# Optimization experiments

Measured on AMD Instinct MI355X. Metric: run time of the kernel, lower is better.

The kernel has to match this reference:

```python
import jax, jax.numpy as jnp
import numpy as np


def _split_box(v):
    # BoxTensor.from_vector: split last dim into (min z, max Z)
    D = v.shape[-1] // 2
    return v[..., :D], v[..., D:]


def setup_inputs() -> dict:
    key = jax.random.key(0)
    k1, k2 = jax.random.split(key)
    men_embeds = jax.random.normal(k1, (256, 128), dtype=jnp.float32)
    all_en_embeds = jax.random.normal(k2, (20000, 128), dtype=jnp.float32)
    return {"men_embeds": men_embeds, "all_en_embeds": all_en_embeds}


def reference(men_embeds, all_en_embeds):
    # men boxes: [M, D] min/max ; entity boxes: [N, D] min/max
    zm, Zm = _split_box(men_embeds)
    ze, Ze = _split_box(all_en_embeds)
    # intersection box per (mention, candidate): [M, N, D]
    lo = jnp.maximum(zm[:, None, :], ze[None, :, :])
    hi = jnp.minimum(Zm[:, None, :], Ze[None, :, :])
    # soft volume: prod_d softplus(side) -> log-volume = sum log softplus
    log_int_vol = jnp.sum(jnp.log(jax.nn.softplus(hi - lo)), axis=-1)   # [M, N]
    log_men_vol = jnp.sum(jnp.log(jax.nn.softplus(Zm - zm)), axis=-1)   # [M]
    # containment log prob = log vol(men ∩ en) - log vol(men); logits = exp(.)
    return jnp.exp(log_int_vol - log_men_vol[:, None])
```

## Files before the change

### kernel.cpp

```cpp
#include <hip/hip_runtime.h>


#define BM 32
#define BN 64
#define DD 64
#define MST 34
#define NST 68
#define CLEN 8
#define NCHUNK 8

__global__ __launch_bounds__(256, 3)
void ivr_kernel(const float* __restrict__ men, const float* __restrict__ en,
                float* __restrict__ out, int M, int N) {
    __shared__ __align__(16) float sEm[DD][MST];
    __shared__ __align__(16) float sIm[DD][MST];
    __shared__ __align__(16) float sEe[DD][NST];
    __shared__ __align__(16) float sIe[DD][NST];
    __shared__ float sRc[NCHUNK][MST];

    const int tx = threadIdx.x;
    const int m0 = blockIdx.y * BM;
    const int n0 = blockIdx.x * BN;

    {
        const int m = tx >> 3;
        const int c = tx & 7;
        int mm = m0 + m; if (mm >= M) mm = M - 1;
        const float* row = men + (size_t)mm * 128;
        float prod = 1.0f;
        #pragma unroll
        for (int k = 0; k < CLEN; ++k) {
            const int d = c * CLEN + k;
            const float Em = __expf(row[DD + d]);
            const float Im = __expf(-row[d]);
            sEm[d][m] = Em;
            sIm[d][m] = Im;
            prod *= __log2f(1.0f + Em * Im);
        }
        sRc[c][m] = 1.0f / prod;
    }
    for (int i = tx; i < BN * DD; i += 256) {
        const int d = i & (DD - 1);
        const int n = i >> 6;
        int nn = n0 + n; if (nn >= N) nn = N - 1;
        sEe[d][n] = __expf(en[(size_t)nn * 128 + DD + d]);
        sIe[d][n] = __expf(-en[(size_t)nn * 128 + d]);
    }
    __syncthreads();

    const int ni = (tx & 15) * 4;
    const int mi = (tx >> 4) * 2;

    float p[2][4];
    #pragma unroll
    for (int i = 0; i < 2; ++i)
        #pragma unroll
        for (int j = 0; j < 4; ++j) p[i][j] = 1.0f;

    #pragma unroll 1
    for (int c = 0; c < NCHUNK; ++c) {
        #pragma unroll
        for (int k = 0; k < CLEN; ++k) {
            const int d = c * CLEN + k;
            const float2 Em2 = *reinterpret_cast<const float2*>(&sEm[d][mi]);
            const float2 Im2 = *reinterpret_cast<const float2*>(&sIm[d][mi]);
            const float4 Ee4 = *reinterpret_cast<const float4*>(&sEe[d][ni]);
            const float4 Ie4 = *reinterpret_cast<const float4*>(&sIe[d][ni]);
            const float EmA[2] = {Em2.x, Em2.y};
            const float ImA[2] = {Im2.x, Im2.y};
            const float EeA[4] = {Ee4.x, Ee4.y, Ee4.z, Ee4.w};
            const float IeA[4] = {Ie4.x, Ie4.y, Ie4.z, Ie4.w};
            #pragma unroll
            for (int i = 0; i < 2; ++i) {
                #pragma unroll
                for (int j = 0; j < 4; ++j) {
                    const float u = fminf(EmA[i], EeA[j]) * fminf(ImA[i], IeA[j]);
                    p[i][j] *= __log2f(1.0f + u);
                }
            }
        }
        const float rc0 = sRc[c][mi];
        const float rc1 = sRc[c][mi + 1];
        #pragma unroll
        for (int j = 0; j < 4; ++j) { p[0][j] *= rc0; p[1][j] *= rc1; }
    }

    #pragma unroll
    for (int i = 0; i < 2; ++i) {
        const int m = m0 + mi + i;
        if (m >= M) continue;
        const int n = n0 + ni;
        if (n + 4 <= N) {
            *reinterpret_cast<float4*>(&out[(size_t)m * N + n]) =
                make_float4(p[i][0], p[i][1], p[i][2], p[i][3]);
        } else {
            #pragma unroll
            for (int j = 0; j < 4; ++j)
                if (n + j < N) out[(size_t)m * N + n + j] = p[i][j];
        }
    }
}

extern "C" void kernel_launch(void* const* d_in, const int* in_sizes, int n_in,
                              void* d_out, int out_size, void* d_ws, size_t ws_size,
                              hipStream_t stream) {
    const float* men = (const float*)d_in[0];
    const float* en  = (const float*)d_in[1];
    float* out = (float*)d_out;
    const int M = in_sizes[0] / 128;
    const int N = in_sizes[1] / 128;
    dim3 grid((N + BN - 1) / BN, (M + BM - 1) / BM);
    ivr_kernel<<<grid, dim3(256), 0, stream>>>(men, en, out, M, N);
}
```

Baseline: 143.3 us.

## Split depth into halves, shrink shared memory, process two N tiles per block

Staging now covers the feature dimension in two halves of 32, which roughly halves shared memory per block, and the launch bounds are raised from 3 to 5 blocks per CU. Each block now loops over two N tiles with a stride, so the grid is about half as wide. Global loads become float4, and log2(1+u) is computed with fmaf. The intent is more occupancy and fewer blocks to launch. The cost is an extra sync pair per half, mention boxes recomputed for every half and tile, and possible register pressure under the tighter bound.

```diff
diff --git a/kernel.cpp b/kernel.cpp
--- a/kernel.cpp
+++ b/kernel.cpp
@@ -3,100 +3,129 @@
 
 #define BM 32
 #define BN 64
-#define DD 64
+#define DH 32
 #define MST 34
-#define NST 68
-#define CLEN 8
-#define NCHUNK 8
+#define NST 66
 
-__global__ __launch_bounds__(256, 3)
+__global__ __launch_bounds__(256, 5)
 void ivr_kernel(const float* __restrict__ men, const float* __restrict__ en,
-                float* __restrict__ out, int M, int N) {
-    __shared__ __align__(16) float sEm[DD][MST];
-    __shared__ __align__(16) float sIm[DD][MST];
-    __shared__ __align__(16) float sEe[DD][NST];
-    __shared__ __align__(16) float sIe[DD][NST];
-    __shared__ float sRc[NCHUNK][MST];
+                float* __restrict__ out, int M, int N, int ntl, int jst) {
+    __shared__ float sEm[DH][MST];
+    __shared__ float sIm[DH][MST];
+    __shared__ float sEe[DH][NST];
+    __shared__ float sIe[DH][NST];
+    __shared__ float sRc[4][MST];
 
     const int tx = threadIdx.x;
     const int m0 = blockIdx.y * BM;
-    const int n0 = blockIdx.x * BN;
-
-    {
-        const int m = tx >> 3;
-        const int c = tx & 7;
-        int mm = m0 + m; if (mm >= M) mm = M - 1;
-        const float* row = men + (size_t)mm * 128;
-        float prod = 1.0f;
-        #pragma unroll
-        for (int k = 0; k < CLEN; ++k) {
-            const int d = c * CLEN + k;
-            const float Em = __expf(row[DD + d]);
-            const float Im = __expf(-row[d]);
-            sEm[d][m] = Em;
-            sIm[d][m] = Im;
-            prod *= __log2f(1.0f + Em * Im);
-        }
-        sRc[c][m] = 1.0f / prod;
-    }
-    for (int i = tx; i < BN * DD; i += 256) {
-        const int d = i & (DD - 1);
-        const int n = i >> 6;
-        int nn = n0 + n; if (nn >= N) nn = N - 1;
-        sEe[d][n] = __expf(en[(size_t)nn * 128 + DD + d]);
-        sIe[d][n] = __expf(-en[(size_t)nn * 128 + d]);
-    }
-    __syncthreads();
+    const int j  = blockIdx.x;
 
     const int ni = (tx & 15) * 4;
     const int mi = (tx >> 4) * 2;
 
-    float p[2][4];
-    #pragma unroll
-    for (int i = 0; i < 2; ++i)
+    const int ntiles = (j + jst < ntl) ? 2 : 1;
+
+    for (int t = 0; t < ntiles; ++t) {
+        const int n0 = (j + t * jst) * BN;
+
+        float p[2][4];
         #pragma unroll
-        for (int j = 0; j < 4; ++j) p[i][j] = 1.0f;
+        for (int i = 0; i < 2; ++i)
+            #pragma unroll
+            for (int jj = 0; jj < 4; ++jj) p[i][jj] = 1.0f;
 
-    #pragma unroll 1
-    for (int c = 0; c < NCHUNK; ++c) {
         #pragma unroll
-        for (int k = 0; k < CLEN; ++k) {
-            const int d = c * CLEN + k;
-            const float2 Em2 = *reinterpret_cast<const float2*>(&sEm[d][mi]);
-            const float2 Im2 = *reinterpret_cast<const float2*>(&sIm[d][mi]);
-            const float4 Ee4 = *reinterpret_cast<const float4*>(&sEe[d][ni]);
-            const float4 Ie4 = *reinterpret_cast<const float4*>(&sIe[d][ni]);
-            const float EmA[2] = {Em2.x, Em2.y};
-            const float ImA[2] = {Im2.x, Im2.y};
-            const float EeA[4] = {Ee4.x, Ee4.y, Ee4.z, Ee4.w};
-            const float IeA[4] = {Ie4.x, Ie4.y, Ie4.z, Ie4.w};
+        for (int h = 0; h < 2; ++h) {
+            const int dofs = h * DH;
+
+            if (tx < 128) {
+                const int m = tx & 31;
+                const int c = tx >> 5;
+                int mm = m0 + m; if (mm >= M) mm = M - 1;
+                const float* row = men + (size_t)mm * 128 + dofs + c * 8;
+                const float4 za = *reinterpret_cast<const float4*>(row);
+                const float4 zb = *reinterpret_cast<const float4*>(row + 4);
+                const float4 Za = *reinterpret_cast<const float4*>(row + 64);
+                const float4 Zb = *reinterpret_cast<const float4*>(row + 68);
+                const float zA[8] = {za.x, za.y, za.z, za.w, zb.x, zb.y, zb.z, zb.w};
+                const float ZA[8] = {Za.x, Za.y, Za.z, Za.w, Zb.x, Zb.y, Zb.z, Zb.w};
+                float prod = 1.0f;
+                #pragma unroll
+                for (int k = 0; k < 8; ++k) {
+                    const int dl = c * 8 + k;
+                    const float Em = __expf(ZA[k]);
+                    const float Im = __expf(-zA[k]);
+                    sEm[dl][m] = Em;
+                    sIm[dl][m] = Im;
+                    prod *= __log2f(fmaf(Em, Im, 1.0f));
+                }
+                sRc[c][m] = 1.0f / prod;
+            }
             #pragma unroll
-            for (int i = 0; i < 2; ++i) {
+            for (int it = 0; it < 2; ++it) {
+                const int q   = tx + it * 256;
+                const int dl4 = (q & 7) * 4;
+                const int n   = q >> 3;
+                int nn = n0 + n; if (nn >= N) nn = N - 1;
+                const float* erow = en + (size_t)nn * 128 + dofs + dl4;
+                const float4 z4 = *reinterpret_cast<const float4*>(erow);
+                const float4 Z4 = *reinterpret_cast<const float4*>(erow + 64);
+                sEe[dl4 + 0][n] = __expf(Z4.x);
+                sEe[dl4 + 1][n] = __expf(Z4.y);
+                sEe[dl4 + 2][n] = __expf(Z4.z);
+                sEe[dl4 + 3][n] = __expf(Z4.w);
+                sIe[dl4 + 0][n] = __expf(-z4.x);
+                sIe[dl4 + 1][n] = __expf(-z4.y);
+                sIe[dl4 + 2][n] = __expf(-z4.z);
+                sIe[dl4 + 3][n] = __expf(-z4.w);
+            }
+            __syncthreads();
+
+            #pragma unroll 1
+            for (int c = 0; c < 4; ++c) {
                 #pragma unroll
-                for (int j = 0; j < 4; ++j) {
-                    const float u = fminf(EmA[i], EeA[j]) * fminf(ImA[i], IeA[j]);
-                    p[i][j] *= __log2f(1.0f + u);
+                for (int k = 0; k < 8; ++k) {
+                    const int dl = c * 8 + k;
+                    const float2 Em2 = *reinterpret_cast<const float2*>(&sEm[dl][mi]);
+                    const float2 Im2 = *reinterpret_cast<const float2*>(&sIm[dl][mi]);
+                    const float2 Ee0 = *reinterpret_cast<const float2*>(&sEe[dl][ni]);
+                    const float2 Ee1 = *reinterpret_cast<const float2*>(&sEe[dl][ni + 2]);
+                    const float2 Ie0 = *reinterpret_cast<const float2*>(&sIe[dl][ni]);
+                    const float2 Ie1 = *reinterpret_cast<const float2*>(&sIe[dl][ni + 2]);
+                    const float EmA[2] = {Em2.x, Em2.y};
+                    const float ImA[2] = {Im2.x, Im2.y};
+                    const float EeA[4] = {Ee0.x, Ee0.y, Ee1.x, Ee1.y};
+                    const float IeA[4] = {Ie0.x, Ie0.y, Ie1.x, Ie1.y};
+                    #pragma unroll
+                    for (int i = 0; i < 2; ++i) {
+                        #pragma unroll
+                        for (int jj = 0; jj < 4; ++jj) {
+                            const float w = fmaf(fminf(EmA[i], EeA[jj]),
+                                                 fminf(ImA[i], IeA[jj]), 1.0f);
+                            p[i][jj] *= __log2f(w);
+                        }
+                    }
                 }
+                const float2 rc = *reinterpret_cast<const float2*>(&sRc[c][mi]);
+                #pragma unroll
+                for (int jj = 0; jj < 4; ++jj) { p[0][jj] *= rc.x; p[1][jj] *= rc.y; }
             }
+            __syncthreads();
         }
-        const float rc0 = sRc[c][mi];
-        const float rc1 = sRc[c][mi + 1];
+
         #pragma unroll
-        for (int j = 0; j < 4; ++j) { p[0][j] *= rc0; p[1][j] *= rc1; }
-    }
-
-    #pragma unroll
-    for (int i = 0; i < 2; ++i) {
-        const int m = m0 + mi + i;
-        if (m >= M) continue;
-        const int n = n0 + ni;
-        if (n + 4 <= N) {
-            *reinterpret_cast<float4*>(&out[(size_t)m * N + n]) =
-                make_float4(p[i][0], p[i][1], p[i][2], p[i][3]);
-        } else {
-            #pragma unroll
-            for (int j = 0; j < 4; ++j)
-                if (n + j < N) out[(size_t)m * N + n + j] = p[i][j];
+        for (int i = 0; i < 2; ++i) {
+            const int m = m0 + mi + i;
+            if (m >= M) continue;
+            const int n = n0 + ni;
+            if (n + 4 <= N) {
+                *reinterpret_cast<float4*>(&out[(size_t)m * N + n]) =
+                    make_float4(p[i][0], p[i][1], p[i][2], p[i][3]);
+            } else {
+                #pragma unroll
+                for (int jj = 0; jj < 4; ++jj)
+                    if (n + jj < N) out[(size_t)m * N + n + jj] = p[i][jj];
+            }
         }
     }
 }
@@ -109,6 +138,8 @@
     float* out = (float*)d_out;
     const int M = in_sizes[0] / 128;
     const int N = in_sizes[1] / 128;
-    dim3 grid((N + BN - 1) / BN, (M + BM - 1) / BM);
-    ivr_kernel<<<grid, dim3(256), 0, stream>>>(men, en, out, M, N);
+    const int ntl = (N + BN - 1) / BN;
+    const int jst = (ntl + 1) / 2;
+    dim3 grid(jst, (M + BM - 1) / BM);
+    ivr_kernel<<<grid, dim3(256), 0, stream>>>(men, en, out, M, N, ntl, jst);
 }
```

New measurement: 149.0 us. +4.0%, slower.

## Precompute exp-transformed boxes in workspace and stream tiles via LDS DMA

Applied to the files above, without the earlier changes.

Adds a pre-pass kernel that computes the exp-transformed entity and mention box bounds once, stored in tile-transposed layout in the workspace, along with the per-chunk reciprocal mention volumes. The main kernel then loads these tiles into shared memory with direct global-to-LDS loads, splits D into two halves to cut shared memory use and allow higher occupancy, and has each block handle two N tiles so mention data is reused. The goal is to stop recomputing exp for every (M-tile, N-tile) pair and to cut global-load latency. In exchange it adds a second launch and workspace traffic, and it falls back to the old kernel when the workspace is too small or M is not a multiple of 32.

```diff
diff --git a/kernel.cpp b/kernel.cpp
--- a/kernel.cpp
+++ b/kernel.cpp
@@ -1,27 +1,192 @@
 #include <hip/hip_runtime.h>
+#include <stdint.h>
 
 
 #define BM 32
 #define BN 64
-#define DD 64
-#define MST 34
-#define NST 68
-#define CLEN 8
-#define NCHUNK 8
+#define DH 32
+
+__device__ __forceinline__ void dma16(const float* g, float* l) {
+    __builtin_amdgcn_global_load_lds(
+        (const __attribute__((address_space(1))) void*)g,
+        (__attribute__((address_space(3))) void*)l, 16, 0, 0);
+}
+
+__global__ __launch_bounds__(256)
+void ivr_pre(const float* __restrict__ men, const float* __restrict__ en,
+             float* __restrict__ ws, int M, int N, int ntl) {
+    float* EeT = ws;
+    float* IeT = EeT + (size_t)ntl * 4096;
+    float* EmT = IeT + (size_t)ntl * 4096;
+    float* ImT = EmT + 16384;
+    float* RcG = ImT + 16384;
+    const int b = blockIdx.x, tx = threadIdx.x;
+    if (b < ntl) {
+        const int n0 = b * BN;
+        #pragma unroll
+        for (int i = 0; i < 8; ++i) {
+            const int q = i * 256 + tx;
+            const int n = q >> 5, c4 = q & 31;
+            int nn = n0 + n; if (nn >= N) nn = N - 1;
+            const float4 v = *reinterpret_cast<const float4*>(en + (size_t)nn * 128 + c4 * 4);
+            const float vv[4] = {v.x, v.y, v.z, v.w};
+            #pragma unroll
+            for (int e = 0; e < 4; ++e) {
+                const int d = c4 * 4 + e;
+                if (d < 64) {
+                    IeT[(size_t)b * 4096 + (d >> 5) * 2048 + (d & 31) * 64 + n] = __expf(-vv[e]);
+                } else {
+                    const int dd = d - 64;
+                    EeT[(size_t)b * 4096 + (dd >> 5) * 2048 + (dd & 31) * 64 + n] = __expf(vv[e]);
+                }
+            }
+        }
+    } else {
+        int m = tx; if (m >= M) m = M - 1;
+        const int mt = m >> 5, ml = m & 31;
+        const float* row = men + (size_t)m * 128;
+        float prod[8];
+        #pragma unroll
+        for (int c = 0; c < 8; ++c) prod[c] = 1.0f;
+        #pragma unroll
+        for (int c4 = 0; c4 < 16; ++c4) {
+            const float4 zv = *reinterpret_cast<const float4*>(row + c4 * 4);
+            const float4 Zv = *reinterpret_cast<const float4*>(row + 64 + c4 * 4);
+            const float zz[4] = {zv.x, zv.y, zv.z, zv.w};
+            const float ZZ[4] = {Zv.x, Zv.y, Zv.z, Zv.w};
+            #pragma unroll
+            for (int e = 0; e < 4; ++e) {
+                const int d = c4 * 4 + e;
+                const float Em = __expf(ZZ[e]);
+                const float Im = __expf(-zz[e]);
+                const int idx = (mt * 2 + (d >> 5)) * 1024 + (d & 31) * 32 + ml;
+                EmT[idx] = Em;
+                ImT[idx] = Im;
+                prod[d >> 3] *= __log2f(fmaf(Em, Im, 1.0f));
+            }
+        }
+        #pragma unroll
+        for (int c = 0; c < 8; ++c)
+            RcG[mt * 256 + c * 32 + ml] = 1.0f / prod[c];
+    }
+}
+
+__global__ __launch_bounds__(256, 6)
+void ivr_main(const float* __restrict__ ws, float* __restrict__ out,
+              int M, int N, int ntl, int jst) {
+    __shared__ __align__(16) float sEe[DH][BN];
+    __shared__ __align__(16) float sIe[DH][BN];
+    __shared__ __align__(16) float sEm[DH][BM];
+    __shared__ __align__(16) float sIm[DH][BM];
+    __shared__ __align__(16) float sRc[8][BM];
+
+    const float* EeT = ws;
+    const float* IeT = EeT + (size_t)ntl * 4096;
+    const float* EmT = IeT + (size_t)ntl * 4096;
+    const float* ImT = EmT + 16384;
+    const float* RcG = ImT + 16384;
+
+    const int tx = threadIdx.x;
+    const int w = tx >> 6, lane = tx & 63;
+    const int mt = blockIdx.y, j = blockIdx.x;
+    const int ntiles = (j + jst < ntl) ? 2 : 1;
+    const int ni = (tx & 15) * 4;
+    const int mi = (tx >> 4) * 2;
+
+    if (w == 0) dma16(RcG + mt * 256 + lane * 4, &sRc[0][0]);
+
+    float p[2][2][4];
+    #pragma unroll
+    for (int t = 0; t < 2; ++t)
+        #pragma unroll
+        for (int i = 0; i < 2; ++i)
+            #pragma unroll
+            for (int jj = 0; jj < 4; ++jj) p[t][i][jj] = 1.0f;
+
+    #pragma unroll 1
+    for (int h = 0; h < 2; ++h) {
+        {
+            const float* gEm = EmT + (mt * 2 + h) * 1024;
+            const float* gIm = ImT + (mt * 2 + h) * 1024;
+            dma16(gEm + w * 256 + lane * 4, &sEm[0][0] + w * 256);
+            dma16(gIm + w * 256 + lane * 4, &sIm[0][0] + w * 256);
+        }
+        for (int t = 0; t < ntiles; ++t) {
+            const int j2 = j + t * jst;
+            const float* gE = EeT + (size_t)j2 * 4096 + h * 2048;
+            const float* gI = IeT + (size_t)j2 * 4096 + h * 2048;
+            const int o = w * 512 + lane * 4;
+            dma16(gE + o,       &sEe[0][0] + w * 512);
+            dma16(gE + o + 256, &sEe[0][0] + w * 512 + 256);
+            dma16(gI + o,       &sIe[0][0] + w * 512);
+            dma16(gI + o + 256, &sIe[0][0] + w * 512 + 256);
+            __syncthreads();
+
+            #pragma unroll 1
+            for (int c = 0; c < 4; ++c) {
+                #pragma unroll
+                for (int k = 0; k < 8; ++k) {
+                    const int dl = c * 8 + k;
+                    const float2 Em2 = *reinterpret_cast<const float2*>(&sEm[dl][mi]);
+                    const float2 Im2 = *reinterpret_cast<const float2*>(&sIm[dl][mi]);
+                    const float4 Ee4 = *reinterpret_cast<const float4*>(&sEe[dl][ni]);
+                    const float4 Ie4 = *reinterpret_cast<const float4*>(&sIe[dl][ni]);
+                    const float EmA[2] = {Em2.x, Em2.y};
+                    const float ImA[2] = {Im2.x, Im2.y};
+                    const float EeA[4] = {Ee4.x, Ee4.y, Ee4.z, Ee4.w};
+                    const float IeA[4] = {Ie4.x, Ie4.y, Ie4.z, Ie4.w};
+                    #pragma unroll
+                    for (int i = 0; i < 2; ++i) {
+                        #pragma unroll
+                        for (int jj = 0; jj < 4; ++jj) {
+                            const float ww = fmaf(fminf(EmA[i], EeA[jj]),
+                                                  fminf(ImA[i], IeA[jj]), 1.0f);
+                            p[t][i][jj] *= __log2f(ww);
+                        }
+                    }
+                }
+                const float2 rc = *reinterpret_cast<const float2*>(&sRc[h * 4 + c][mi]);
+                #pragma unroll
+                for (int jj = 0; jj < 4; ++jj) { p[t][0][jj] *= rc.x; p[t][1][jj] *= rc.y; }
+            }
+            __syncthreads();
+        }
+    }
+
+    for (int t = 0; t < ntiles; ++t) {
+        const int n0 = (j + t * jst) * BN;
+        #pragma unroll
+        for (int i = 0; i < 2; ++i) {
+            const int m = mt * BM + mi + i;
+            if (m >= M) continue;
+            const int n = n0 + ni;
+            if (n + 4 <= N) {
+                *reinterpret_cast<float4*>(&out[(size_t)m * N + n]) =
+                    make_float4(p[t][i][0], p[t][i][1], p[t][i][2], p[t][i][3]);
+            } else {
+                #pragma unroll
+                for (int jj = 0; jj < 4; ++jj)
+                    if (n + jj < N) out[(size_t)m * N + n + jj] = p[t][i][jj];
+            }
+        }
+    }
+}
+
+#define FB_MST 34
+#define FB_NST 68
 
 __global__ __launch_bounds__(256, 3)
-void ivr_kernel(const float* __restrict__ men, const float* __restrict__ en,
-                float* __restrict__ out, int M, int N) {
-    __shared__ __align__(16) float sEm[DD][MST];
-    __shared__ __align__(16) float sIm[DD][MST];
-    __shared__ __align__(16) float sEe[DD][NST];
-    __shared__ __align__(16) float sIe[DD][NST];
-    __shared__ float sRc[NCHUNK][MST];
+void ivr_fb(const float* __restrict__ men, const float* __restrict__ en,
+            float* __restrict__ out, int M, int N) {
+    __shared__ __align__(16) float sEm[64][FB_MST];
+    __shared__ __align__(16) float sIm[64][FB_MST];
+    __shared__ __align__(16) float sEe[64][FB_NST];
+    __shared__ __align__(16) float sIe[64][FB_NST];
+    __shared__ float sRc[8][FB_MST];
 
     const int tx = threadIdx.x;
     const int m0 = blockIdx.y * BM;
     const int n0 = blockIdx.x * BN;
-
     {
         const int m = tx >> 3;
         const int c = tx & 7;
@@ -29,62 +194,61 @@
         const float* row = men + (size_t)mm * 128;
         float prod = 1.0f;
         #pragma unroll
-        for (int k = 0; k < CLEN; ++k) {
-            const int d = c * CLEN + k;
-            const float Em = __expf(row[DD + d]);
+        for (int k = 0; k < 8; ++k) {
+            const int d = c * 8 + k;
+            const float Em = __expf(row[64 + d]);
             const float Im = __expf(-row[d]);
             sEm[d][m] = Em;
             sIm[d][m] = Im;
-            prod *= __log2f(1.0f + Em * Im);
+            prod *= __log2f(fmaf(Em, Im, 1.0f));
         }
         sRc[c][m] = 1.0f / prod;
     }
-    for (int i = tx; i < BN * DD; i += 256) {
-        const int d = i & (DD - 1);
+    for (int i = tx; i < BN * 64; i += 256) {
+        const int d = i & 63;
         const int n = i >> 6;
         int nn = n0 + n; if (nn >= N) nn = N - 1;
-        sEe[d][n] = __expf(en[(size_t)nn * 128 + DD + d]);
+        sEe[d][n] = __expf(en[(size_t)nn * 128 + 64 + d]);
         sIe[d][n] = __expf(-en[(size_t)nn * 128 + d]);
     }
     __syncthreads();
 
     const int ni = (tx & 15) * 4;
     const int mi = (tx >> 4) * 2;
-
     float p[2][4];
     #pragma unroll
     for (int i = 0; i < 2; ++i)
         #pragma unroll
-        for (int j = 0; j < 4; ++j) p[i][j] = 1.0f;
+        for (int jj = 0; jj < 4; ++jj) p[i][jj] = 1.0f;
 
     #pragma unroll 1
-    for (int c = 0; c < NCHUNK; ++c) {
-        #pragma unroll
-        for (int k = 0; k < CLEN; ++k) {
-            const int d = c * CLEN + k;
+    for (int c = 0; c < 8; ++c) {
+        #pragma unroll
+        for (int k = 0; k < 8; ++k) {
+            const int d = c * 8 + k;
             const float2 Em2 = *reinterpret_cast<const float2*>(&sEm[d][mi]);
             const float2 Im2 = *reinterpret_cast<const float2*>(&sIm[d][mi]);
-            const float4 Ee4 = *reinterpret_cast<const float4*>(&sEe[d][ni]);
-            const float4 Ie4 = *reinterpret_cast<const float4*>(&sIe[d][ni]);
+            const float2 Ee0 = *reinterpret_cast<const float2*>(&sEe[d][ni]);
+            const float2 Ee1 = *reinterpret_cast<const float2*>(&sEe[d][ni + 2]);
+            const float2 Ie0 = *reinterpret_cast<const float2*>(&sIe[d][ni]);
+            const float2 Ie1 = *reinterpret_cast<const float2*>(&sIe[d][ni + 2]);
             const float EmA[2] = {Em2.x, Em2.y};
             const float ImA[2] = {Im2.x, Im2.y};
-            const float EeA[4] = {Ee4.x, Ee4.y, Ee4.z, Ee4.w};
-            const float IeA[4] = {Ie4.x, Ie4.y, Ie4.z, Ie4.w};
-            #pragma unroll
-            for (int i = 0; i < 2; ++i) {
-                #pragma unroll
-                for (int j = 0; j < 4; ++j) {
-                    const float u = fminf(EmA[i], EeA[j]) * fminf(ImA[i], IeA[j]);
-                    p[i][j] *= __log2f(1.0f + u);
+            const float EeA[4] = {Ee0.x, Ee0.y, Ee1.x, Ee1.y};
+            const float IeA[4] = {Ie0.x, Ie0.y, Ie1.x, Ie1.y};
+            #pragma unroll
+            for (int i = 0; i < 2; ++i)
+                #pragma unroll
+                for (int jj = 0; jj < 4; ++jj) {
+                    const float ww = fmaf(fminf(EmA[i], EeA[jj]),
+                                          fminf(ImA[i], IeA[jj]), 1.0f);
+                    p[i][jj] *= __log2f(ww);
                 }
-            }
-        }
-        const float rc0 = sRc[c][mi];
-        const float rc1 = sRc[c][mi + 1];
-        #pragma unroll
-        for (int j = 0; j < 4; ++j) { p[0][j] *= rc0; p[1][j] *= rc1; }
-    }
-
+        }
+        const float2 rc = *reinterpret_cast<const float2*>(&sRc[c][mi]);
+        #pragma unroll
+        for (int jj = 0; jj < 4; ++jj) { p[0][jj] *= rc.x; p[1][jj] *= rc.y; }
+    }
     #pragma unroll
     for (int i = 0; i < 2; ++i) {
         const int m = m0 + mi + i;
@@ -95,8 +259,8 @@
                 make_float4(p[i][0], p[i][1], p[i][2], p[i][3]);
         } else {
             #pragma unroll
-            for (int j = 0; j < 4; ++j)
-                if (n + j < N) out[(size_t)m * N + n + j] = p[i][j];
+            for (int jj = 0; jj < 4; ++jj)
+                if (n + jj < N) out[(size_t)m * N + n + jj] = p[i][jj];
         }
     }
 }
@@ -109,6 +273,13 @@
     float* out = (float*)d_out;
     const int M = in_sizes[0] / 128;
     const int N = in_sizes[1] / 128;
-    dim3 grid((N + BN - 1) / BN, (M + BM - 1) / BM);
-    ivr_kernel<<<grid, dim3(256), 0, stream>>>(men, en, out, M, N);
-}
+    const int ntl = (N + BN - 1) / BN;
+    const int jst = (ntl + 1) / 2;
+    const size_t need = ((size_t)2 * ntl * 4096 + 2 * 16384 + 2048) * sizeof(float);
+    if (ws_size >= need && (M & 31) == 0) {
+        ivr_pre<<<dim3(ntl + 1), dim3(256), 0, stream>>>(men, en, (float*)d_ws, M, N, ntl);
+        ivr_main<<<dim3(jst, M / BM), dim3(256), 0, stream>>>((const float*)d_ws, out, M, N, ntl, jst);
+    } else {
+        ivr_fb<<<dim3(ntl, (M + BM - 1) / BM), dim3(256), 0, stream>>>(men, en, out, M, N);
+    }
+}
```

Result: slower. 167.0 us (+16.5%).

## Bound intersections in fp16, zero negligible outputs, and compute only survivors exactly

Applied to the files above, without the earlier changes.

Replaces the single dense kernel with three passes. A stats pass computes per-mention reciprocal volumes and a cutoff. A cheap packed-fp16 bound pass sums the clipped side lengths per (mention, entity) pair and writes zeros. Pairs whose concavity-based upper bound exceeds the cutoff are appended to an atomic queue in workspace, and an exact pass recomputes only those pairs in fp32. This avoids the transcendental-heavy log/softplus work for the many pairs whose result is negligibly small. The cost is two extra launches, an atomic queue, and a silent cap on queue size. Outputs below roughly 2^-43.5 become exact zeros, and fp16 rounding could slightly loosen the bound.

```diff
diff --git a/kernel.cpp b/kernel.cpp
--- a/kernel.cpp
+++ b/kernel.cpp
@@ -1,103 +1,293 @@
 #include <hip/hip_runtime.h>
+#include <stdint.h>
 
 
 #define BM 32
 #define BN 64
-#define DD 64
-#define MST 34
-#define NST 68
-#define CLEN 8
-#define NCHUNK 8
-
-__global__ __launch_bounds__(256, 3)
-void ivr_kernel(const float* __restrict__ men, const float* __restrict__ en,
-                float* __restrict__ out, int M, int N) {
-    __shared__ __align__(16) float sEm[DD][MST];
-    __shared__ __align__(16) float sIm[DD][MST];
-    __shared__ __align__(16) float sEe[DD][NST];
-    __shared__ __align__(16) float sIe[DD][NST];
-    __shared__ float sRc[NCHUNK][MST];
+#define CUT 43.5f
+#define QOFF 9232
+
+typedef _Float16 h2 __attribute__((ext_vector_type(2)));
+typedef _Float16 h4 __attribute__((ext_vector_type(4)));
+
+__global__ __launch_bounds__(256)
+void ivr_stats(const float* __restrict__ men, float* __restrict__ ws, int M) {
+    const int tx = threadIdx.x;
+    if (tx == 0) *((unsigned*)ws) = 0u;
+    float* Cm  = (float*)((char*)ws + 16);
+    float* rcM = Cm + 256;
+    if (tx >= M) return;
+    const float* row = men + (size_t)tx * 128;
+    float Lm = 0.f;
+    for (int c = 0; c < 8; ++c) {
+        float prod = 1.f;
+        #pragma unroll
+        for (int k = 0; k < 8; ++k) {
+            const int d = c * 8 + k;
+            const float u = __expf(row[64 + d] - row[d]);
+            const float w = 1.f + u;
+            float l2 = __log2f(w);
+            if (u < 0.5f) l2 += (u - (w - 1.f)) * 1.44269504f;
+            prod *= l2;
+            Lm += __log2f(l2 * 0.69314718f);
+        }
+        rcM[tx * 8 + c] = 1.f / prod;
+    }
+    const float V = exp2f((Lm - CUT) * (1.f / 64.f));
+    Cm[tx] = 64.f * __logf(expm1f(V));
+}
+
+__global__ __launch_bounds__(256, 4)
+void ivr_bound(const float* __restrict__ men, const float* __restrict__ en,
+               float* __restrict__ out, float* __restrict__ ws,
+               int M, int N, unsigned qcap) {
+    __shared__ _Float16 sEZ[64][68];
+    __shared__ _Float16 sEz[64][68];
+    __shared__ _Float16 sMZ[64][68];
+    __shared__ _Float16 sMz[64][68];
 
     const int tx = threadIdx.x;
     const int m0 = blockIdx.y * BM;
     const int n0 = blockIdx.x * BN;
+    const float* Cm = (const float*)((const char*)ws + 16);
+    unsigned* qcount = (unsigned*)ws;
+    unsigned* queue  = (unsigned*)((char*)ws + QOFF);
 
     {
-        const int m = tx >> 3;
-        const int c = tx & 7;
+        const int nq = tx & 15;
+        const int db = (tx >> 4) * 4;
+        const float* er[4];
+        #pragma unroll
+        for (int k = 0; k < 4; ++k) {
+            int nn = n0 + nq * 4 + k; if (nn >= N) nn = N - 1;
+            er[k] = en + (size_t)nn * 128;
+        }
+        #pragma unroll
+        for (int j = 0; j < 4; ++j) {
+            const int d = db + j;
+            h4 hz, hZ;
+            #pragma unroll
+            for (int k = 0; k < 4; ++k) {
+                hz[k] = (_Float16)er[k][d];
+                hZ[k] = (_Float16)er[k][64 + d];
+            }
+            *(h4*)&sEz[d][nq * 4] = hz;
+            *(h4*)&sEZ[d][nq * 4] = hZ;
+        }
+    }
+    {
+        const int m = tx & 31;
+        const int db8 = (tx >> 5) * 8;
         int mm = m0 + m; if (mm >= M) mm = M - 1;
         const float* row = men + (size_t)mm * 128;
-        float prod = 1.0f;
-        #pragma unroll
-        for (int k = 0; k < CLEN; ++k) {
-            const int d = c * CLEN + k;
-            const float Em = __expf(row[DD + d]);
-            const float Im = __expf(-row[d]);
-            sEm[d][m] = Em;
-            sIm[d][m] = Im;
-            prod *= __log2f(1.0f + Em * Im);
-        }
-        sRc[c][m] = 1.0f / prod;
-    }
-    for (int i = tx; i < BN * DD; i += 256) {
-        const int d = i & (DD - 1);
-        const int n = i >> 6;
-        int nn = n0 + n; if (nn >= N) nn = N - 1;
-        sEe[d][n] = __expf(en[(size_t)nn * 128 + DD + d]);
-        sIe[d][n] = __expf(-en[(size_t)nn * 128 + d]);
+        #pragma unroll
+        for (int k = 0; k < 8; ++k) {
+            const int d = db8 + k;
+            const _Float16 vz = (_Float16)row[d];
+            const _Float16 vZ = (_Float16)row[64 + d];
+            *(h2*)&sMz[d][2 * m] = (h2){vz, vz};
+            *(h2*)&sMZ[d][2 * m] = (h2){vZ, vZ};
+        }
     }
     __syncthreads();
 
-    const int ni = (tx & 15) * 4;
-    const int mi = (tx >> 4) * 2;
-
-    float p[2][4];
+    const int tn = tx & 15, tm = tx >> 4;
+    const int ni = tn * 4, mi = tm * 2;
+
+    float acc[2][4];
     #pragma unroll
     for (int i = 0; i < 2; ++i)
         #pragma unroll
-        for (int j = 0; j < 4; ++j) p[i][j] = 1.0f;
+        for (int j = 0; j < 4; ++j) acc[i][j] = 0.f;
 
     #pragma unroll 1
-    for (int c = 0; c < NCHUNK; ++c) {
-        #pragma unroll
-        for (int k = 0; k < CLEN; ++k) {
-            const int d = c * CLEN + k;
-            const float2 Em2 = *reinterpret_cast<const float2*>(&sEm[d][mi]);
-            const float2 Im2 = *reinterpret_cast<const float2*>(&sIm[d][mi]);
-            const float4 Ee4 = *reinterpret_cast<const float4*>(&sEe[d][ni]);
-            const float4 Ie4 = *reinterpret_cast<const float4*>(&sIe[d][ni]);
-            const float EmA[2] = {Em2.x, Em2.y};
-            const float ImA[2] = {Im2.x, Im2.y};
-            const float EeA[4] = {Ee4.x, Ee4.y, Ee4.z, Ee4.w};
-            const float IeA[4] = {Ie4.x, Ie4.y, Ie4.z, Ie4.w};
+    for (int c = 0; c < 8; ++c) {
+        h2 ca[2][2];
+        ca[0][0] = ca[0][1] = ca[1][0] = ca[1][1] = (h2)(_Float16)0;
+        #pragma unroll
+        for (int k = 0; k < 8; ++k) {
+            const int d = c * 8 + k;
+            const h4 eZ = *(const h4*)&sEZ[d][ni];
+            const h4 ez = *(const h4*)&sEz[d][ni];
+            const h4 mZ = *(const h4*)&sMZ[d][2 * mi];
+            const h4 mz = *(const h4*)&sMz[d][2 * mi];
             #pragma unroll
             for (int i = 0; i < 2; ++i) {
-                #pragma unroll
-                for (int j = 0; j < 4; ++j) {
-                    const float u = fminf(EmA[i], EeA[j]) * fminf(ImA[i], IeA[j]);
-                    p[i][j] *= __log2f(1.0f + u);
+                const h2 mZ2 = i ? mZ.zw : mZ.xy;
+                const h2 mz2 = i ? mz.zw : mz.xy;
+                ca[i][0] = ca[i][0] +
+                    (__builtin_elementwise_min(eZ.xy, mZ2) -
+                     __builtin_elementwise_max(ez.xy, mz2));
+                ca[i][1] = ca[i][1] +
+                    (__builtin_elementwise_min(eZ.zw, mZ2) -
+                     __builtin_elementwise_max(ez.zw, mz2));
+            }
+        }
+        #pragma unroll
+        for (int i = 0; i < 2; ++i) {
+            acc[i][0] += (float)ca[i][0].x;  acc[i][1] += (float)ca[i][0].y;
+            acc[i][2] += (float)ca[i][1].x;  acc[i][3] += (float)ca[i][1].y;
+        }
+    }
+
+    const float cm0 = Cm[m0 + mi], cm1 = Cm[m0 + mi + 1];
+
+    #pragma unroll
+    for (int i = 0; i < 2; ++i) {
+        const int m = m0 + mi + i;
+        const int n = n0 + ni;
+        if (m < M) {
+            if (n + 4 <= N)
+                *(float4*)&out[(size_t)m * N + n] = make_float4(0.f, 0.f, 0.f, 0.f);
+            else
+                for (int j = 0; j < 4; ++j) if (n + j < N) out[(size_t)m * N + n + j] = 0.f;
+        }
+    }
+    const int lane = tx & 63;
+    #pragma unroll
+    for (int i = 0; i < 2; ++i) {
+        const int m = m0 + mi + i;
+        const float cmv = i ? cm1 : cm0;
+        #pragma unroll
+        for (int j = 0; j < 4; ++j) {
+            const int n = n0 + ni + j;
+            const bool flag = (acc[i][j] >= cmv) && (n < N) && (m < M);
+            const unsigned long long mask = __ballot(flag);
+            if (mask) {
+                const int lead = (int)__ffsll(mask) - 1;
+                unsigned base = 0;
+                if (lane == lead) base = atomicAdd(qcount, (unsigned)__popcll(mask));
+                base = (unsigned)__shfl((int)base, lead, 64);
+                if (flag) {
+                    const unsigned off =
+                        (unsigned)__popcll(mask & ((1ull << lane) - 1ull));
+                    const unsigned idx = base + off;
+                    if (idx < qcap) queue[idx] = ((unsigned)m << 16) | (unsigned)n;
                 }
             }
         }
-        const float rc0 = sRc[c][mi];
-        const float rc1 = sRc[c][mi + 1];
-        #pragma unroll
-        for (int j = 0; j < 4; ++j) { p[0][j] *= rc0; p[1][j] *= rc1; }
-    }
-
+    }
+}
+
+__global__ __launch_bounds__(256)
+void ivr_exact(const float* __restrict__ men, const float* __restrict__ en,
+               float* __restrict__ out, const float* __restrict__ ws,
+               int N, unsigned qcap) {
+    const unsigned nq0 = *((const unsigned*)ws);
+    const unsigned nq = nq0 < qcap ? nq0 : qcap;
+    const float* rcM = (const float*)((const char*)ws + 16) + 256;
+    const unsigned* queue = (const unsigned*)((const char*)ws + QOFF);
+    for (unsigned idx = blockIdx.x * 256 + threadIdx.x; idx < nq;
+         idx += gridDim.x * 256) {
+        const unsigned id = queue[idx];
+        const int m = (int)(id >> 16), n = (int)(id & 0xFFFFu);
+        const float* mr = men + (size_t)m * 128;
+        const float* er = en + (size_t)n * 128;
+        float p = 1.f;
+        #pragma unroll 1
+        for (int c = 0; c < 8; ++c) {
+            float q = 1.f;
+            #pragma unroll
+            for (int h = 0; h < 2; ++h) {
+                const int d0 = c * 8 + h * 4;
+                const float4 zm4 = *(const float4*)(mr + d0);
+                const float4 Zm4 = *(const float4*)(mr + 64 + d0);
+                const float4 ze4 = *(const float4*)(er + d0);
+                const float4 Ze4 = *(const float4*)(er + 64 + d0);
+                const float zmA[4] = {zm4.x, zm4.y, zm4.z, zm4.w};
+                const float ZmA[4] = {Zm4.x, Zm4.y, Zm4.z, Zm4.w};
+                const float zeA[4] = {ze4.x, ze4.y, ze4.z, ze4.w};
+                const float ZeA[4] = {Ze4.x, Ze4.y, Ze4.z, Ze4.w};
+                #pragma unroll
+                for (int e = 0; e < 4; ++e) {
+                    const float t = fminf(ZmA[e], ZeA[e]) - fmaxf(zmA[e], zeA[e]);
+                    const float u = __expf(t);
+                    q *= __log2f(1.f + u);
+                }
+            }
+            p *= q * rcM[m * 8 + c];
+        }
+        out[(size_t)m * N + n] = p;
+    }
+}
+
+#define FB_MST 34
+#define FB_NST 68
+__global__ __launch_bounds__(256, 3)
+void ivr_fb(const float* __restrict__ men, const float* __restrict__ en,
+            float* __restrict__ out, int M, int N) {
+    __shared__ __align__(16) float sEm[64][FB_MST];
+    __shared__ __align__(16) float sIm[64][FB_MST];
+    __shared__ __align__(16) float sEe[64][FB_NST];
+    __shared__ __align__(16) float sIe[64][FB_NST];
+    __shared__ float sRc[8][FB_MST];
+    const int tx = threadIdx.x;
+    const int m0 = blockIdx.y * BM;
+    const int n0 = blockIdx.x * BN;
+    {
+        const int m = tx >> 3, c = tx & 7;
+        int mm = m0 + m; if (mm >= M) mm = M - 1;
+        const float* row = men + (size_t)mm * 128;
+        float prod = 1.f;
+        #pragma unroll
+        for (int k = 0; k < 8; ++k) {
+            const int d = c * 8 + k;
+            const float Em = __expf(row[64 + d]);
+            const float Im = __expf(-row[d]);
+            sEm[d][m] = Em; sIm[d][m] = Im;
+            prod *= __log2f(fmaf(Em, Im, 1.f));
+        }
+        sRc[c][m] = 1.f / prod;
+    }
+    for (int i = tx; i < BN * 64; i += 256) {
+        const int d = i & 63, n = i >> 6;
+        int nn = n0 + n; if (nn >= N) nn = N - 1;
+        sEe[d][n] = __expf(en[(size_t)nn * 128 + 64 + d]);
+        sIe[d][n] = __expf(-en[(size_t)nn * 128 + d]);
+    }
+    __syncthreads();
+    const int ni = (tx & 15) * 4, mi = (tx >> 4) * 2;
+    float p[2][4];
+    #pragma unroll
+    for (int i = 0; i < 2; ++i)
+        #pragma unroll
+        for (int jj = 0; jj < 4; ++jj) p[i][jj] = 1.f;
+    #pragma unroll 1
+    for (int c = 0; c < 8; ++c) {
+        #pragma unroll
+        for (int k = 0; k < 8; ++k) {
+            const int d = c * 8 + k;
+            const float2 Em2 = *(const float2*)&sEm[d][mi];
+            const float2 Im2 = *(const float2*)&sIm[d][mi];
+            const float2 Ee0 = *(const float2*)&sEe[d][ni];
+            const float2 Ee1 = *(const float2*)&sEe[d][ni + 2];
+            const float2 Ie0 = *(const float2*)&sIe[d][ni];
+            const float2 Ie1 = *(const float2*)&sIe[d][ni + 2];
+            const float EmA[2] = {Em2.x, Em2.y}, ImA[2] = {Im2.x, Im2.y};
+            const float EeA[4] = {Ee0.x, Ee0.y, Ee1.x, Ee1.y};
+            const float IeA[4] = {Ie0.x, Ie0.y, Ie1.x, Ie1.y};
+            #pragma unroll
+            for (int i = 0; i < 2; ++i)
+                #pragma unroll
+                for (int jj = 0; jj < 4; ++jj) {
+                    const float ww = fmaf(fminf(EmA[i], EeA[jj]),
+                                          fminf(ImA[i], IeA[jj]), 1.f);
+                    p[i][jj] *= __log2f(ww);
+                }
+        }
+        const float2 rc = *(const float2*)&sRc[c][mi];
+        #pragma unroll
+        for (int jj = 0; jj < 4; ++jj) { p[0][jj] *= rc.x; p[1][jj] *= rc.y; }
+    }
     #pragma unroll
     for (int i = 0; i < 2; ++i) {
         const int m = m0 + mi + i;
         if (m >= M) continue;
         const int n = n0 + ni;
-        if (n + 4 <= N) {
-            *reinterpret_cast<float4*>(&out[(size_t)m * N + n]) =
-                make_float4(p[i][0], p[i][1], p[i][2], p[i][3]);
-        } else {
-            #pragma unroll
-            for (int j = 0; j < 4; ++j)
-                if (n + j < N) out[(size_t)m * N + n + j] = p[i][j];
-        }
+        if (n + 4 <= N) *(float4*)&out[(size_t)m * N + n] =
+            make_float4(p[i][0], p[i][1], p[i][2], p[i][3]);
+        else for (int jj = 0; jj < 4; ++jj)
+            if (n + jj < N) out[(size_t)m * N + n + jj] = p[i][jj];
     }
 }
 
@@ -109,6 +299,16 @@
     float* out = (float*)d_out;
     const int M = in_sizes[0] / 128;
     const int N = in_sizes[1] / 128;
-    dim3 grid((N + BN - 1) / BN, (M + BM - 1) / BM);
-    ivr_kernel<<<grid, dim3(256), 0, stream>>>(men, en, out, M, N);
-}
+    const int ntl = (N + BN - 1) / BN;
+    const int mtl = (M + BM - 1) / BM;
+    if (M <= 256 && N < 65536 && ws_size >= (size_t)(QOFF + (1u << 20))) {
+        const unsigned qcap = (unsigned)((ws_size - QOFF) / 4);
+        ivr_stats<<<1, 256, 0, stream>>>(men, (float*)d_ws, M);
+        ivr_bound<<<dim3(ntl, mtl), 256, 0, stream>>>(men, en, out, (float*)d_ws,
+                                                      M, N, qcap);
+        ivr_exact<<<128, 256, 0, stream>>>(men, en, out, (const float*)d_ws,
+                                           N, qcap);
+    } else {
+        ivr_fb<<<dim3(ntl, mtl), 256, 0, stream>>>(men, en, out, M, N);
+    }
+}
```

Result: slower. 215.4 us (+50.3%).
